# Kernel optimization log

Hardware: AMD Instinct MI355X
Metric: run time of the kernel (lower is better)

The kernel has to match this reference:

```python
import jax, jax.numpy as jnp
import numpy as np

N, E = 50000, 1600000
NODE_F, EDGE_F = 128, 64
H, F = 4, 16
NEG_SLOPE = 0.2


def setup_inputs() -> dict:
    key = jax.random.key(0)
    ks = jax.random.split(key, 12)
    return {
        "nfeat": jax.random.normal(ks[0], (N, NODE_F), jnp.float32),
        "efeat": jax.random.normal(ks[1], (E, EDGE_F), jnp.float32),
        "W_node": jax.random.normal(ks[2], (NODE_F, H * F), jnp.float32) * 0.1,
        "b_node": jax.random.normal(ks[3], (H * F,), jnp.float32) * 0.1,
        "W_edge": jax.random.normal(ks[4], (EDGE_F, H * F), jnp.float32) * 0.1,
        "b_edge": jax.random.normal(ks[5], (H * F,), jnp.float32) * 0.1,
        "attn_l": jax.random.normal(ks[6], (H, F), jnp.float32) * 0.1,
        "attn_r": jax.random.normal(ks[7], (H, F), jnp.float32) * 0.1,
        "attn_e": jax.random.normal(ks[8], (H, F), jnp.float32) * 0.1,
        "src": jax.random.randint(ks[9], (E,), 0, N, jnp.int32),
        "dst": jax.random.randint(ks[10], (E,), 0, N, jnp.int32),
    }


def reference(nfeat, efeat, W_node, b_node, W_edge, b_edge,
              attn_l, attn_r, attn_e, src, dst):
    n = nfeat.shape[0]
    node_feat = (nfeat @ W_node + b_node).reshape(n, H, F)   # [N,H,F]
    edge_feat = (efeat @ W_edge + b_edge).reshape(-1, H, F)  # [E,H,F]
    el = jnp.einsum('nhf,hf->nh', node_feat, attn_l)  # [N,H]
    er = jnp.einsum('nhf,hf->nh', node_feat, attn_r)  # [N,H]
    ee = jnp.einsum('ehf,hf->eh', edge_feat, attn_e)  # [E,H]
    el_prime = el[src] + ee                            # u_add_e, [E,H]
    e = el_prime + er[dst]                             # e_add_v, [E,H]
    e = jnp.where(e > 0, e, NEG_SLOPE * e)             # leaky_relu
    # edge softmax over incoming edges per destination node
    emax = jax.ops.segment_max(e, dst, num_segments=n)      # [N,H]
    ex = jnp.exp(e - emax[dst])                              # [E,H]
    denom = jax.ops.segment_sum(ex, dst, num_segments=n)    # [N,H]
    a = ex / denom[dst]                                      # [E,H]
    # msg_fn: a * el_prime (scalar per edge/head) -> scatter-sum to dst
    m = a * el_prime                                          # [E,H]
    rst = jax.ops.segment_sum(m, dst, num_segments=n)        # [N,H]
    return rst[..., None]                                     # [N,H,1]
```

## Files before the change

### kernel.cpp

```cpp
#include <hip/hip_runtime.h>

constexpr int H = 4;
constexpr int F = 16;
constexpr int NODE_F = 128;
constexpr int EDGE_F = 64;
constexpr float NEG_SLOPE = 0.2f;

__global__ void fold_kernel(const float* __restrict__ Wn, const float* __restrict__ bn,
                            const float* __restrict__ Wed, const float* __restrict__ bed,
                            const float* __restrict__ al, const float* __restrict__ ar,
                            const float* __restrict__ ae,
                            float* __restrict__ Wl, float* __restrict__ Wr,
                            float* __restrict__ We, float* __restrict__ bv,
                            int* __restrict__ total) {
    int idx = threadIdx.x;
    if (idx == 0) *total = 0;
    if (idx < NODE_F * H) {
        int k = idx >> 2, h = idx & 3;
        float sl = 0.f, sr = 0.f;
        #pragma unroll
        for (int f = 0; f < F; ++f) {
            float w = Wn[k * (H * F) + h * F + f];
            sl += w * al[h * F + f];
            sr += w * ar[h * F + f];
        }
        Wl[idx] = sl; Wr[idx] = sr;
    }
    if (idx < EDGE_F * H) {
        int k = idx >> 2, h = idx & 3;
        float s = 0.f;
        #pragma unroll
        for (int f = 0; f < F; ++f) s += Wed[k * (H * F) + h * F + f] * ae[h * F + f];
        We[idx] = s;
    }
    if (idx < H) {
        float sl = 0.f, sr = 0.f, se = 0.f;
        #pragma unroll
        for (int f = 0; f < F; ++f) {
            sl += bn[idx * F + f] * al[idx * F + f];
            sr += bn[idx * F + f] * ar[idx * F + f];
            se += bed[idx * F + f] * ae[idx * F + f];
        }
        bv[idx] = sl; bv[H + idx] = sr; bv[2 * H + idx] = se;
    }
}

__global__ void node_proj_kernel(const float* __restrict__ nfeat,
                                 const float* __restrict__ Wl, const float* __restrict__ Wr,
                                 const float* __restrict__ bv,
                                 float* __restrict__ el, float* __restrict__ er,
                                 int* __restrict__ deg, int N) {
    __shared__ float sWl[NODE_F * H];
    __shared__ float sWr[NODE_F * H];
    for (int i = threadIdx.x; i < NODE_F * H; i += blockDim.x) { sWl[i] = Wl[i]; sWr[i] = Wr[i]; }
    __syncthreads();
    int lane = threadIdx.x & 63;
    int wave = (int)(((size_t)blockIdx.x * blockDim.x + threadIdx.x) >> 6);
    int sub = lane & 3, ln = lane >> 2;
    int n = wave * 16 + ln;
    if (n >= N) return;
    float accl[H] = {0.f, 0.f, 0.f, 0.f};
    float accr[H] = {0.f, 0.f, 0.f, 0.f};
    const float4* row = (const float4*)(nfeat + (size_t)n * NODE_F);
    #pragma unroll
    for (int i = 0; i < 8; ++i) {
        float4 v = row[sub + 4 * i];
        int k0 = (sub + 4 * i) * 4;
        #pragma unroll
        for (int h = 0; h < H; ++h) {
            accl[h] += v.x * sWl[(k0 + 0) * H + h] + v.y * sWl[(k0 + 1) * H + h]
                     + v.z * sWl[(k0 + 2) * H + h] + v.w * sWl[(k0 + 3) * H + h];
            accr[h] += v.x * sWr[(k0 + 0) * H + h] + v.y * sWr[(k0 + 1) * H + h]
                     + v.z * sWr[(k0 + 2) * H + h] + v.w * sWr[(k0 + 3) * H + h];
        }
    }
    #pragma unroll
    for (int m = 1; m < 4; m <<= 1) {
        #pragma unroll
        for (int h = 0; h < H; ++h) {
            accl[h] += __shfl_xor(accl[h], m);
            accr[h] += __shfl_xor(accr[h], m);
        }
    }
    el[(size_t)n * H + sub] = accl[sub] + bv[sub];
    er[(size_t)n * H + sub] = accr[sub] + bv[H + sub];
    if (sub == 0) deg[n] = 0;
}

__global__ void edge_proj_kernel(const float* __restrict__ efeat,
                                 const int* __restrict__ src, const int* __restrict__ dst,
                                 const float* __restrict__ We, const float* __restrict__ bv,
                                 const float* __restrict__ el,
                                 float* __restrict__ payload, int* __restrict__ idx,
                                 int* __restrict__ deg, int E) {
    __shared__ float sWe[EDGE_F * H];
    __shared__ float sbe[H];
    for (int i = threadIdx.x; i < EDGE_F * H; i += blockDim.x) sWe[i] = We[i];
    if (threadIdx.x < H) sbe[threadIdx.x] = bv[2 * H + threadIdx.x];
    __syncthreads();
    int lane = threadIdx.x & 63;
    int wave = (int)(((size_t)blockIdx.x * blockDim.x + threadIdx.x) >> 6);
    int sub = lane & 3, le = lane >> 2;
    int e = wave * 16 + le;
    if (e >= E) return;
    float acc[H] = {0.f, 0.f, 0.f, 0.f};
    const float4* row = (const float4*)(efeat + (size_t)e * EDGE_F);
    #pragma unroll
    for (int i = 0; i < 4; ++i) {
        float4 v = row[sub + 4 * i];
        int k0 = (sub + 4 * i) * 4;
        #pragma unroll
        for (int h = 0; h < H; ++h) {
            acc[h] += v.x * sWe[(k0 + 0) * H + h] + v.y * sWe[(k0 + 1) * H + h]
                    + v.z * sWe[(k0 + 2) * H + h] + v.w * sWe[(k0 + 3) * H + h];
        }
    }
    #pragma unroll
    for (int m = 1; m < 4; m <<= 1) {
        #pragma unroll
        for (int h = 0; h < H; ++h) acc[h] += __shfl_xor(acc[h], m);
    }
    int s = src[e];
    payload[(size_t)e * H + sub] = el[(size_t)s * H + sub] + acc[sub] + sbe[sub];
    if (sub == 0) idx[e] = atomicAdd(deg + dst[e], 1);
}

__global__ void offsets_kernel(const int* __restrict__ deg, int* __restrict__ off,
                               int* __restrict__ total, int N) {
    int lane = threadIdx.x & 63;
    int gid = blockIdx.x * blockDim.x + threadIdx.x;
    int x = (gid < N) ? deg[gid] : 0;
    int incl = x;
    #pragma unroll
    for (int s = 1; s < 64; s <<= 1) {
        int y = __shfl_up(incl, s);
        if (lane >= s) incl += y;
    }
    int wtot = __shfl(incl, 63);
    int base = 0;
    if (lane == 63) base = atomicAdd(total, wtot);
    base = __shfl(base, 63);
    if (gid < N) off[gid] = base + incl - x;
}

__global__ void scatter_eid_kernel(const int* __restrict__ dst, const int* __restrict__ idx,
                                   const int* __restrict__ off, int* __restrict__ eid, int E) {
    int e = blockIdx.x * blockDim.x + threadIdx.x;
    if (e >= E) return;
    eid[off[dst[e]] + idx[e]] = e;
}

__global__ void node_reduce_kernel(const float* __restrict__ payload,
                                   const int* __restrict__ eid,
                                   const int* __restrict__ off, const int* __restrict__ deg,
                                   const float* __restrict__ er,
                                   float* __restrict__ out, int N) {
    int lane = threadIdx.x & 63;
    int wave = (int)(((size_t)blockIdx.x * blockDim.x + threadIdx.x) >> 6);
    int g = lane >> 4;
    int gl = lane & 15;
    int n = wave * 4 + g;
    if (n >= N) return;
    int o = off[n], dg = deg[n];
    float4 erv = *(const float4*)(er + (size_t)n * H);
    float n0 = 0.f, n1 = 0.f, n2 = 0.f, n3 = 0.f;
    float d0 = 0.f, d1 = 0.f, d2 = 0.f, d3 = 0.f;
    for (int i = gl; i < dg; i += 16) {
        int ee = eid[o + i];
        float4 p = *(const float4*)(payload + (size_t)ee * H);
        float e0 = p.x + erv.x, e1 = p.y + erv.y, e2 = p.z + erv.z, e3 = p.w + erv.w;
        e0 = e0 > 0.f ? e0 : NEG_SLOPE * e0;
        e1 = e1 > 0.f ? e1 : NEG_SLOPE * e1;
        e2 = e2 > 0.f ? e2 : NEG_SLOPE * e2;
        e3 = e3 > 0.f ? e3 : NEG_SLOPE * e3;
        float x0 = expf(e0), x1 = expf(e1), x2 = expf(e2), x3 = expf(e3);
        n0 += x0 * p.x; n1 += x1 * p.y; n2 += x2 * p.z; n3 += x3 * p.w;
        d0 += x0; d1 += x1; d2 += x2; d3 += x3;
    }
    #pragma unroll
    for (int s = 8; s; s >>= 1) {
        n0 += __shfl_down(n0, s, 16); n1 += __shfl_down(n1, s, 16);
        n2 += __shfl_down(n2, s, 16); n3 += __shfl_down(n3, s, 16);
        d0 += __shfl_down(d0, s, 16); d1 += __shfl_down(d1, s, 16);
        d2 += __shfl_down(d2, s, 16); d3 += __shfl_down(d3, s, 16);
    }
    if (gl == 0) {
        *(float4*)(out + (size_t)n * H) =
            make_float4(d0 > 0.f ? n0 / d0 : 0.f, d1 > 0.f ? n1 / d1 : 0.f,
                        d2 > 0.f ? n2 / d2 : 0.f, d3 > 0.f ? n3 / d3 : 0.f);
    }
}

__global__ void zero_kernel(float* __restrict__ p, int n) {
    int i = blockIdx.x * blockDim.x + threadIdx.x;
    if (i < n) p[i] = 0.f;
}

__global__ void edge_atomic_kernel(const float* __restrict__ efeat,
                                   const int* __restrict__ src, const int* __restrict__ dst,
                                   const float* __restrict__ We, const float* __restrict__ bv,
                                   const float* __restrict__ el, const float* __restrict__ er,
                                   float* __restrict__ num, float* __restrict__ den, int E) {
    __shared__ float sWe[EDGE_F * H];
    __shared__ float sbe[H];
    for (int i = threadIdx.x; i < EDGE_F * H; i += blockDim.x) sWe[i] = We[i];
    if (threadIdx.x < H) sbe[threadIdx.x] = bv[2 * H + threadIdx.x];
    __syncthreads();
    int e = blockIdx.x * blockDim.x + threadIdx.x;
    if (e >= E) return;
    float acc[H] = {sbe[0], sbe[1], sbe[2], sbe[3]};
    const float4* row = (const float4*)(efeat + (size_t)e * EDGE_F);
    #pragma unroll
    for (int j = 0; j < EDGE_F / 4; ++j) {
        float4 v = row[j];
        #pragma unroll
        for (int h = 0; h < H; ++h) {
            acc[h] += v.x * sWe[(4 * j + 0) * H + h] + v.y * sWe[(4 * j + 1) * H + h]
                    + v.z * sWe[(4 * j + 2) * H + h] + v.w * sWe[(4 * j + 3) * H + h];
        }
    }
    int s = src[e], d = dst[e];
    float4 elv = *(const float4*)(el + (size_t)s * H);
    float4 erv = *(const float4*)(er + (size_t)d * H);
    float p0 = elv.x + acc[0], p1 = elv.y + acc[1], p2 = elv.z + acc[2], p3 = elv.w + acc[3];
    float e0 = p0 + erv.x, e1 = p1 + erv.y, e2 = p2 + erv.z, e3 = p3 + erv.w;
    e0 = e0 > 0.f ? e0 : NEG_SLOPE * e0;
    e1 = e1 > 0.f ? e1 : NEG_SLOPE * e1;
    e2 = e2 > 0.f ? e2 : NEG_SLOPE * e2;
    e3 = e3 > 0.f ? e3 : NEG_SLOPE * e3;
    float x0 = expf(e0), x1 = expf(e1), x2 = expf(e2), x3 = expf(e3);
    float* nb = num + (size_t)d * H;
    float* db = den + (size_t)d * H;
    atomicAdd(nb + 0, x0 * p0); atomicAdd(nb + 1, x1 * p1);
    atomicAdd(nb + 2, x2 * p2); atomicAdd(nb + 3, x3 * p3);
    atomicAdd(db + 0, x0); atomicAdd(db + 1, x1);
    atomicAdd(db + 2, x2); atomicAdd(db + 3, x3);
}

__global__ void finalize_kernel(const float* __restrict__ num, const float* __restrict__ den,
                                float* __restrict__ out, int NH) {
    int i = blockIdx.x * blockDim.x + threadIdx.x;
    if (i < NH) {
        float d = den[i];
        out[i] = d > 0.f ? num[i] / d : 0.f;
    }
}

extern "C" void kernel_launch(void* const* d_in, const int* in_sizes, int n_in,
                              void* d_out, int out_size, void* d_ws, size_t ws_size,
                              hipStream_t stream) {
    const float* nfeat = (const float*)d_in[0];
    const float* efeat = (const float*)d_in[1];
    const float* Wn    = (const float*)d_in[2];
    const float* bn    = (const float*)d_in[3];
    const float* Wed   = (const float*)d_in[4];
    const float* bed   = (const float*)d_in[5];
    const float* al    = (const float*)d_in[6];
    const float* ar    = (const float*)d_in[7];
    const float* ae    = (const float*)d_in[8];
    const int*   src   = (const int*)d_in[9];
    const int*   dst   = (const int*)d_in[10];

    int N = in_sizes[0] / NODE_F;
    int E = in_sizes[1] / EDGE_F;
    float* out = (float*)d_out;
    float* ws  = (float*)d_ws;

    size_t p_payload = 0;
    size_t p_el   = p_payload + (size_t)E * 4;
    size_t p_er   = p_el + (size_t)N * H;
    size_t p_Wl   = p_er + (size_t)N * H;
    size_t p_Wr   = p_Wl + 512;
    size_t p_We   = p_Wr + 512;
    size_t p_bv   = p_We + 256;
    size_t p_tot  = p_bv + 16;
    size_t p_deg  = p_tot + 16;
    size_t p_off  = p_deg + (size_t)N;
    size_t p_idx  = p_off + (size_t)N;
    size_t p_eid  = p_idx + (size_t)E;
    size_t csr_total = (p_eid + (size_t)E) * sizeof(float);

    if (ws_size >= csr_total) {
        float* payload = ws + p_payload;
        float* el = ws + p_el;
        float* er = ws + p_er;
        float* Wl = ws + p_Wl;
        float* Wr = ws + p_Wr;
        float* We = ws + p_We;
        float* bv = ws + p_bv;
        int* total = (int*)(ws + p_tot);
        int* deg = (int*)(ws + p_deg);
        int* off = (int*)(ws + p_off);
        int* idx = (int*)(ws + p_idx);
        int* eid = (int*)(ws + p_eid);

        fold_kernel<<<1, 512, 0, stream>>>(Wn, bn, Wed, bed, al, ar, ae, Wl, Wr, We, bv, total);
        node_proj_kernel<<<(int)(((size_t)N * 4 + 255) / 256), 256, 0, stream>>>(
            nfeat, Wl, Wr, bv, el, er, deg, N);
        edge_proj_kernel<<<(int)(((size_t)E * 4 + 255) / 256), 256, 0, stream>>>(
            efeat, src, dst, We, bv, el, payload, idx, deg, E);
        offsets_kernel<<<(N + 255) / 256, 256, 0, stream>>>(deg, off, total, N);
        scatter_eid_kernel<<<(E + 255) / 256, 256, 0, stream>>>(dst, idx, off, eid, E);
        node_reduce_kernel<<<(int)(((size_t)N * 16 + 255) / 256), 256, 0, stream>>>(
            payload, eid, off, deg, er, out, N);
    } else {
        float* el  = ws;
        float* er  = el + (size_t)N * H;
        float* num = er + (size_t)N * H;
        float* den = num + (size_t)N * H;
        float* Wl  = den + (size_t)N * H;
        float* Wr  = Wl + 512;
        float* We  = Wr + 512;
        float* bv  = We + 256;
        int* total = (int*)(bv + 16);
        int* deg   = total + 16;

        fold_kernel<<<1, 512, 0, stream>>>(Wn, bn, Wed, bed, al, ar, ae, Wl, Wr, We, bv, total);
        node_proj_kernel<<<(int)(((size_t)N * 4 + 255) / 256), 256, 0, stream>>>(
            nfeat, Wl, Wr, bv, el, er, deg, N);
        zero_kernel<<<(int)(((size_t)N * 2 * H + 255) / 256), 256, 0, stream>>>(num, N * 2 * H);
        edge_atomic_kernel<<<(E + 255) / 256, 256, 0, stream>>>(efeat, src, dst, We, bv,
                                                                el, er, num, den, E);
        finalize_kernel<<<(N * H + 255) / 256, 256, 0, stream>>>(num, den, out, N * H);
    }
}
```

Measured before the change: 180.0 us.

## Fold weights into node projection, store fp16 payload, nontemporal eid scatter

Removes the separate single-block fold launch by having every node-projection block recompute the folded attention weights in shared memory, with block 0 also writing the edge weight fold. The per-edge payload is packed as four fp16 values, halving its write and gather traffic, and one lane per edge now writes it. The eid scatter uses nontemporal stores, and the fallback path merges zeroing into its projection kernel. The fp16 payload reduces precision of the logits and messages, and the redundant per-block fold adds compute to each block.

```diff
diff --git a/kernel.cpp b/kernel.cpp
--- a/kernel.cpp
+++ b/kernel.cpp
@@ -1,4 +1,5 @@
 #include <hip/hip_runtime.h>
+#include <hip/hip_fp16.h>
 
 constexpr int H = 4;
 constexpr int F = 16;
@@ -6,17 +7,20 @@
 constexpr int EDGE_F = 64;
 constexpr float NEG_SLOPE = 0.2f;
 
-__global__ void fold_kernel(const float* __restrict__ Wn, const float* __restrict__ bn,
-                            const float* __restrict__ Wed, const float* __restrict__ bed,
-                            const float* __restrict__ al, const float* __restrict__ ar,
-                            const float* __restrict__ ae,
-                            float* __restrict__ Wl, float* __restrict__ Wr,
-                            float* __restrict__ We, float* __restrict__ bv,
-                            int* __restrict__ total) {
-    int idx = threadIdx.x;
-    if (idx == 0) *total = 0;
-    if (idx < NODE_F * H) {
-        int k = idx >> 2, h = idx & 3;
+__global__ void node_proj_kernel(const float* __restrict__ nfeat,
+                                 const float* __restrict__ Wn, const float* __restrict__ bn,
+                                 const float* __restrict__ Wed, const float* __restrict__ bed,
+                                 const float* __restrict__ al, const float* __restrict__ ar,
+                                 const float* __restrict__ ae,
+                                 float* __restrict__ el, float* __restrict__ er,
+                                 float* __restrict__ Weg, float* __restrict__ beg,
+                                 int* __restrict__ total, int* __restrict__ deg, int N) {
+    __shared__ float sWl[NODE_F * H];
+    __shared__ float sWr[NODE_F * H];
+    __shared__ float sbl[H];
+    __shared__ float sbr[H];
+    for (int i = threadIdx.x; i < NODE_F * H; i += blockDim.x) {
+        int k = i >> 2, h = i & 3;
         float sl = 0.f, sr = 0.f;
         #pragma unroll
         for (int f = 0; f < F; ++f) {
@@ -24,35 +28,35 @@
             sl += w * al[h * F + f];
             sr += w * ar[h * F + f];
         }
-        Wl[idx] = sl; Wr[idx] = sr;
-    }
-    if (idx < EDGE_F * H) {
-        int k = idx >> 2, h = idx & 3;
-        float s = 0.f;
-        #pragma unroll
-        for (int f = 0; f < F; ++f) s += Wed[k * (H * F) + h * F + f] * ae[h * F + f];
-        We[idx] = s;
-    }
-    if (idx < H) {
-        float sl = 0.f, sr = 0.f, se = 0.f;
+        sWl[i] = sl; sWr[i] = sr;
+    }
+    if (threadIdx.x < H) {
+        int h = threadIdx.x;
+        float bl = 0.f, br = 0.f;
         #pragma unroll
         for (int f = 0; f < F; ++f) {
-            sl += bn[idx * F + f] * al[idx * F + f];
-            sr += bn[idx * F + f] * ar[idx * F + f];
-            se += bed[idx * F + f] * ae[idx * F + f];
-        }
-        bv[idx] = sl; bv[H + idx] = sr; bv[2 * H + idx] = se;
-    }
-}
-
-__global__ void node_proj_kernel(const float* __restrict__ nfeat,
-                                 const float* __restrict__ Wl, const float* __restrict__ Wr,
-                                 const float* __restrict__ bv,
-                                 float* __restrict__ el, float* __restrict__ er,
-                                 int* __restrict__ deg, int N) {
-    __shared__ float sWl[NODE_F * H];
-    __shared__ float sWr[NODE_F * H];
-    for (int i = threadIdx.x; i < NODE_F * H; i += blockDim.x) { sWl[i] = Wl[i]; sWr[i] = Wr[i]; }
+            bl += bn[h * F + f] * al[h * F + f];
+            br += bn[h * F + f] * ar[h * F + f];
+        }
+        sbl[h] = bl; sbr[h] = br;
+    }
+    if (blockIdx.x == 0) {
+        for (int i = threadIdx.x; i < EDGE_F * H; i += blockDim.x) {
+            int k = i >> 2, h = i & 3;
+            float s = 0.f;
+            #pragma unroll
+            for (int f = 0; f < F; ++f) s += Wed[k * (H * F) + h * F + f] * ae[h * F + f];
+            Weg[i] = s;
+        }
+        if (threadIdx.x < H) {
+            int h = threadIdx.x;
+            float se = 0.f;
+            #pragma unroll
+            for (int f = 0; f < F; ++f) se += bed[h * F + f] * ae[h * F + f];
+            beg[h] = se;
+        }
+        if (threadIdx.x == 0) *total = 0;
+    }
     __syncthreads();
     int lane = threadIdx.x & 63;
     int wave = (int)(((size_t)blockIdx.x * blockDim.x + threadIdx.x) >> 6);
@@ -82,21 +86,21 @@
             accr[h] += __shfl_xor(accr[h], m);
         }
     }
-    el[(size_t)n * H + sub] = accl[sub] + bv[sub];
-    er[(size_t)n * H + sub] = accr[sub] + bv[H + sub];
+    el[(size_t)n * H + sub] = accl[sub] + sbl[sub];
+    er[(size_t)n * H + sub] = accr[sub] + sbr[sub];
     if (sub == 0) deg[n] = 0;
 }
 
 __global__ void edge_proj_kernel(const float* __restrict__ efeat,
                                  const int* __restrict__ src, const int* __restrict__ dst,
-                                 const float* __restrict__ We, const float* __restrict__ bv,
+                                 const float* __restrict__ Weg, const float* __restrict__ beg,
                                  const float* __restrict__ el,
-                                 float* __restrict__ payload, int* __restrict__ idx,
+                                 uint2* __restrict__ pay, int* __restrict__ idx,
                                  int* __restrict__ deg, int E) {
     __shared__ float sWe[EDGE_F * H];
     __shared__ float sbe[H];
-    for (int i = threadIdx.x; i < EDGE_F * H; i += blockDim.x) sWe[i] = We[i];
-    if (threadIdx.x < H) sbe[threadIdx.x] = bv[2 * H + threadIdx.x];
+    for (int i = threadIdx.x; i < EDGE_F * H; i += blockDim.x) sWe[i] = Weg[i];
+    if (threadIdx.x < H) sbe[threadIdx.x] = beg[threadIdx.x];
     __syncthreads();
     int lane = threadIdx.x & 63;
     int wave = (int)(((size_t)blockIdx.x * blockDim.x + threadIdx.x) >> 6);
@@ -120,9 +124,21 @@
         #pragma unroll
         for (int h = 0; h < H; ++h) acc[h] += __shfl_xor(acc[h], m);
     }
-    int s = src[e];
-    payload[(size_t)e * H + sub] = el[(size_t)s * H + sub] + acc[sub] + sbe[sub];
-    if (sub == 0) idx[e] = atomicAdd(deg + dst[e], 1);
+    if (sub == 0) {
+        int s = src[e];
+        float4 elv = *(const float4*)(el + (size_t)s * H);
+        float p0 = elv.x + acc[0] + sbe[0];
+        float p1 = elv.y + acc[1] + sbe[1];
+        float p2 = elv.z + acc[2] + sbe[2];
+        float p3 = elv.w + acc[3] + sbe[3];
+        __half2 a = __floats2half2_rn(p0, p1);
+        __half2 b = __floats2half2_rn(p2, p3);
+        uint2 w;
+        w.x = *(unsigned int*)&a;
+        w.y = *(unsigned int*)&b;
+        pay[e] = w;
+        idx[e] = atomicAdd(deg + dst[e], 1);
+    }
 }
 
 __global__ void offsets_kernel(const int* __restrict__ deg, int* __restrict__ off,
@@ -147,10 +163,10 @@
                                    const int* __restrict__ off, int* __restrict__ eid, int E) {
     int e = blockIdx.x * blockDim.x + threadIdx.x;
     if (e >= E) return;
-    eid[off[dst[e]] + idx[e]] = e;
-}
-
-__global__ void node_reduce_kernel(const float* __restrict__ payload,
+    __builtin_nontemporal_store(e, &eid[off[dst[e]] + idx[e]]);
+}
+
+__global__ void node_reduce_kernel(const uint2* __restrict__ pay,
                                    const int* __restrict__ eid,
                                    const int* __restrict__ off, const int* __restrict__ deg,
                                    const float* __restrict__ er,
@@ -166,15 +182,16 @@
     float n0 = 0.f, n1 = 0.f, n2 = 0.f, n3 = 0.f;
     float d0 = 0.f, d1 = 0.f, d2 = 0.f, d3 = 0.f;
     for (int i = gl; i < dg; i += 16) {
-        int ee = eid[o + i];
-        float4 p = *(const float4*)(payload + (size_t)ee * H);
-        float e0 = p.x + erv.x, e1 = p.y + erv.y, e2 = p.z + erv.z, e3 = p.w + erv.w;
+        uint2 w = pay[eid[o + i]];
+        float2 f01 = __half22float2(*(const __half2*)&w.x);
+        float2 f23 = __half22float2(*(const __half2*)&w.y);
+        float e0 = f01.x + erv.x, e1 = f01.y + erv.y, e2 = f23.x + erv.z, e3 = f23.y + erv.w;
         e0 = e0 > 0.f ? e0 : NEG_SLOPE * e0;
         e1 = e1 > 0.f ? e1 : NEG_SLOPE * e1;
         e2 = e2 > 0.f ? e2 : NEG_SLOPE * e2;
         e3 = e3 > 0.f ? e3 : NEG_SLOPE * e3;
         float x0 = expf(e0), x1 = expf(e1), x2 = expf(e2), x3 = expf(e3);
-        n0 += x0 * p.x; n1 += x1 * p.y; n2 += x2 * p.z; n3 += x3 * p.w;
+        n0 += x0 * f01.x; n1 += x1 * f01.y; n2 += x2 * f23.x; n3 += x3 * f23.y;
         d0 += x0; d1 += x1; d2 += x2; d3 += x3;
     }
     #pragma unroll
@@ -191,9 +208,76 @@
     }
 }
 
-__global__ void zero_kernel(float* __restrict__ p, int n) {
-    int i = blockIdx.x * blockDim.x + threadIdx.x;
-    if (i < n) p[i] = 0.f;
+__global__ void fold_kernel(const float* __restrict__ Wn, const float* __restrict__ bn,
+                            const float* __restrict__ Wed, const float* __restrict__ bed,
+                            const float* __restrict__ al, const float* __restrict__ ar,
+                            const float* __restrict__ ae,
+                            float* __restrict__ Wl, float* __restrict__ Wr,
+                            float* __restrict__ We, float* __restrict__ bv) {
+    int idx = threadIdx.x;
+    if (idx < NODE_F * H) {
+        int k = idx >> 2, h = idx & 3;
+        float sl = 0.f, sr = 0.f;
+        #pragma unroll
+        for (int f = 0; f < F; ++f) {
+            float w = Wn[k * (H * F) + h * F + f];
+            sl += w * al[h * F + f];
+            sr += w * ar[h * F + f];
+        }
+        Wl[idx] = sl; Wr[idx] = sr;
+    }
+    if (idx < EDGE_F * H) {
+        int k = idx >> 2, h = idx & 3;
+        float s = 0.f;
+        #pragma unroll
+        for (int f = 0; f < F; ++f) s += Wed[k * (H * F) + h * F + f] * ae[h * F + f];
+        We[idx] = s;
+    }
+    if (idx < H) {
+        float sl = 0.f, sr = 0.f, se = 0.f;
+        #pragma unroll
+        for (int f = 0; f < F; ++f) {
+            sl += bn[idx * F + f] * al[idx * F + f];
+            sr += bn[idx * F + f] * ar[idx * F + f];
+            se += bed[idx * F + f] * ae[idx * F + f];
+        }
+        bv[idx] = sl; bv[H + idx] = sr; bv[2 * H + idx] = se;
+    }
+}
+
+__global__ void node_proj_fb_kernel(const float* __restrict__ nfeat,
+                                    const float* __restrict__ Wl, const float* __restrict__ Wr,
+                                    const float* __restrict__ bv,
+                                    float* __restrict__ el, float* __restrict__ er,
+                                    float* __restrict__ num, float* __restrict__ den, int N) {
+    __shared__ float sWl[NODE_F * H];
+    __shared__ float sWr[NODE_F * H];
+    for (int i = threadIdx.x; i < NODE_F * H; i += blockDim.x) { sWl[i] = Wl[i]; sWr[i] = Wr[i]; }
+    __syncthreads();
+    int n = blockIdx.x * blockDim.x + threadIdx.x;
+    if (n >= N) return;
+    float accl[H] = {0.f, 0.f, 0.f, 0.f};
+    float accr[H] = {0.f, 0.f, 0.f, 0.f};
+    const float4* row = (const float4*)(nfeat + (size_t)n * NODE_F);
+    #pragma unroll
+    for (int j = 0; j < NODE_F / 4; ++j) {
+        float4 v = row[j];
+        #pragma unroll
+        for (int h = 0; h < H; ++h) {
+            accl[h] += v.x * sWl[(4 * j + 0) * H + h] + v.y * sWl[(4 * j + 1) * H + h]
+                     + v.z * sWl[(4 * j + 2) * H + h] + v.w * sWl[(4 * j + 3) * H + h];
+            accr[h] += v.x * sWr[(4 * j + 0) * H + h] + v.y * sWr[(4 * j + 1) * H + h]
+                     + v.z * sWr[(4 * j + 2) * H + h] + v.w * sWr[(4 * j + 3) * H + h];
+        }
+    }
+    size_t base = (size_t)n * H;
+    #pragma unroll
+    for (int h = 0; h < H; ++h) {
+        el[base + h] = accl[h] + bv[h];
+        er[base + h] = accr[h] + bv[H + h];
+        num[base + h] = 0.f;
+        den[base + h] = 0.f;
+    }
 }
 
 __global__ void edge_atomic_kernel(const float* __restrict__ efeat,
@@ -266,14 +350,12 @@
     float* out = (float*)d_out;
     float* ws  = (float*)d_ws;
 
-    size_t p_payload = 0;
-    size_t p_el   = p_payload + (size_t)E * 4;
+    size_t p_pay  = 0;
+    size_t p_el   = p_pay + (size_t)E * 2;
     size_t p_er   = p_el + (size_t)N * H;
-    size_t p_Wl   = p_er + (size_t)N * H;
-    size_t p_Wr   = p_Wl + 512;
-    size_t p_We   = p_Wr + 512;
-    size_t p_bv   = p_We + 256;
-    size_t p_tot  = p_bv + 16;
+    size_t p_Weg  = p_er + (size_t)N * H;
+    size_t p_beg  = p_Weg + 256;
+    size_t p_tot  = p_beg + 16;
     size_t p_deg  = p_tot + 16;
     size_t p_off  = p_deg + (size_t)N;
     size_t p_idx  = p_off + (size_t)N;
@@ -281,28 +363,25 @@
     size_t csr_total = (p_eid + (size_t)E) * sizeof(float);
 
     if (ws_size >= csr_total) {
-        float* payload = ws + p_payload;
-        float* el = ws + p_el;
-        float* er = ws + p_er;
-        float* Wl = ws + p_Wl;
-        float* Wr = ws + p_Wr;
-        float* We = ws + p_We;
-        float* bv = ws + p_bv;
+        uint2* pay = (uint2*)(ws + p_pay);
+        float* el  = ws + p_el;
+        float* er  = ws + p_er;
+        float* Weg = ws + p_Weg;
+        float* beg = ws + p_beg;
         int* total = (int*)(ws + p_tot);
-        int* deg = (int*)(ws + p_deg);
-        int* off = (int*)(ws + p_off);
-        int* idx = (int*)(ws + p_idx);
-        int* eid = (int*)(ws + p_eid);
-
-        fold_kernel<<<1, 512, 0, stream>>>(Wn, bn, Wed, bed, al, ar, ae, Wl, Wr, We, bv, total);
+        int* deg   = (int*)(ws + p_deg);
+        int* off   = (int*)(ws + p_off);
+        int* idx   = (int*)(ws + p_idx);
+        int* eid   = (int*)(ws + p_eid);
+
         node_proj_kernel<<<(int)(((size_t)N * 4 + 255) / 256), 256, 0, stream>>>(
-            nfeat, Wl, Wr, bv, el, er, deg, N);
+            nfeat, Wn, bn, Wed, bed, al, ar, ae, el, er, Weg, beg, total, deg, N);
         edge_proj_kernel<<<(int)(((size_t)E * 4 + 255) / 256), 256, 0, stream>>>(
-            efeat, src, dst, We, bv, el, payload, idx, deg, E);
+            efeat, src, dst, Weg, beg, el, pay, idx, deg, E);
         offsets_kernel<<<(N + 255) / 256, 256, 0, stream>>>(deg, off, total, N);
         scatter_eid_kernel<<<(E + 255) / 256, 256, 0, stream>>>(dst, idx, off, eid, E);
         node_reduce_kernel<<<(int)(((size_t)N * 16 + 255) / 256), 256, 0, stream>>>(
-            payload, eid, off, deg, er, out, N);
+            pay, eid, off, deg, er, out, N);
     } else {
         float* el  = ws;
         float* er  = el + (size_t)N * H;
@@ -312,13 +391,10 @@
         float* Wr  = Wl + 512;
         float* We  = Wr + 512;
         float* bv  = We + 256;
-        int* total = (int*)(bv + 16);
-        int* deg   = total + 16;
-
-        fold_kernel<<<1, 512, 0, stream>>>(Wn, bn, Wed, bed, al, ar, ae, Wl, Wr, We, bv, total);
-        node_proj_kernel<<<(int)(((size_t)N * 4 + 255) / 256), 256, 0, stream>>>(
-            nfeat, Wl, Wr, bv, el, er, deg, N);
-        zero_kernel<<<(int)(((size_t)N * 2 * H + 255) / 256), 256, 0, stream>>>(num, N * 2 * H);
+
+        fold_kernel<<<1, 512, 0, stream>>>(Wn, bn, Wed, bed, al, ar, ae, Wl, Wr, We, bv);
+        node_proj_fb_kernel<<<(N + 255) / 256, 256, 0, stream>>>(nfeat, Wl, Wr, bv,
+                                                                 el, er, num, den, N);
         edge_atomic_kernel<<<(E + 255) / 256, 256, 0, stream>>>(efeat, src, dst, We, bv,
                                                                 el, er, num, den, E);
         finalize_kernel<<<(N * H + 255) / 256, 256, 0, stream>>>(num, den, out, N * H);
```

Result: slower. 196.6 us (+9.2%).
